# Optimization experiments

Measured on AMD Instinct MI355X. Metric: run time of the kernel, lower is better.

The kernel has to match this reference:

```python
import jax, jax.numpy as jnp
import numpy as np

B, T, H, IN, OUT = 256, 1024, 512, 2, 2


def setup_inputs() -> dict:
    key = jax.random.key(0)
    ks = jax.random.split(key, 12)
    s = 1.0 / np.sqrt(H)
    return {
        "X0": jax.random.normal(ks[0], (B, OUT), jnp.float32),
        "V": jax.random.normal(ks[1], (B, T, IN), jnp.float32),
        # GRU params (torch layout: gates ordered r, z, n)
        "W_ih": jax.random.uniform(ks[2], (3 * H, IN), jnp.float32, -s, s),
        "W_hh": jax.random.uniform(ks[3], (3 * H, H), jnp.float32, -s, s),
        "b_ih": jax.random.uniform(ks[4], (3 * H,), jnp.float32, -s, s),
        "b_hh": jax.random.uniform(ks[5], (3 * H,), jnp.float32, -s, s),
        # attention MLP: Linear(OUT+IN, H//2) -> ReLU -> Linear(H//2, OUT) -> Softmax
        "Wa1": jax.random.uniform(ks[6], (H // 2, OUT + IN), jnp.float32, -s, s),
        "ba1": jax.random.uniform(ks[7], (H // 2,), jnp.float32, -s, s),
        "Wa2": jax.random.uniform(ks[8], (OUT, H // 2), jnp.float32, -s, s),
        "ba2": jax.random.uniform(ks[9], (OUT,), jnp.float32, -s, s),
        # residual layer: Linear(H, OUT)
        "Wr": jax.random.uniform(ks[10], (OUT, H), jnp.float32, -s, s),
        "br": jax.random.uniform(ks[11], (OUT,), jnp.float32, -s, s),
    }


def _forward(X0, V, W_ih, W_hh, b_ih, b_hh, Wa1, ba1, Wa2, ba2, Wr, br):
    # ---- GRU over time (batch_first input, h0 = 0) ----
    # Precompute input projections for all steps: [B, T, 3H]
    gx_all = jnp.einsum('bti,gi->btg', V, W_ih) + b_ih
    gx_tm = jnp.swapaxes(gx_all, 0, 1)  # [T, B, 3H]

    def gru_step(h, gx):
        gh = h @ W_hh.T + b_hh  # [B, 3H]
        r = jax.nn.sigmoid(gx[:, :H] + gh[:, :H])
        z = jax.nn.sigmoid(gx[:, H:2 * H] + gh[:, H:2 * H])
        n = jnp.tanh(gx[:, 2 * H:] + r * gh[:, 2 * H:])
        h_new = (1.0 - z) * n + z * h
        return h_new, h_new

    h0 = jnp.zeros((V.shape[0], H), V.dtype)
    _, h_seq = jax.lax.scan(gru_step, h0, gx_tm)  # [T, B, H]

    # residual_raw = residual_layer(h_t), precomputed for all t: [T, B, OUT]
    res_all = jnp.einsum('tbh,oh->tbo', h_seq, Wr) + br

    v_tm = jnp.swapaxes(V, 0, 1)  # [T, B, IN]; IN == OUT so slice is identity

    def corr_step(x_prev, inp):
        v_t, res_t = inp
        att_in = jnp.concatenate([x_prev, v_t[:, :OUT]], axis=-1)  # [B, OUT+IN]
        hid = jax.nn.relu(att_in @ Wa1.T + ba1)
        aw = jax.nn.softmax(hid @ Wa2.T + ba2, axis=-1)  # [B, OUT]
        x_t = x_prev + v_t[:, :OUT] + aw * res_t
        return x_t, x_t

    _, x_seq = jax.lax.scan(corr_step, X0, (v_tm, res_all))  # [T, B, OUT]
    return jnp.swapaxes(x_seq, 0, 1)  # [B, T, OUT]


def reference(X0, V, W_ih, W_hh, b_ih, b_hh, Wa1, ba1, Wa2, ba2, Wr, br):
    return _forward(X0, V, W_ih, W_hh, b_ih, b_hh, Wa1, ba1, Wa2, ba2, Wr, br)
```

## Files before the change

kernel.cpp:

```cpp
#include <hip/hip_runtime.h>


typedef short bf16x8 __attribute__((ext_vector_type(8)));
typedef float f32x4  __attribute__((ext_vector_type(4)));
typedef unsigned u32x2 __attribute__((ext_vector_type(2)));
typedef unsigned u32x4 __attribute__((ext_vector_type(4)));

__device__ __forceinline__ unsigned f2bf(float f) {
  unsigned u = __builtin_bit_cast(unsigned, f);
  return (u + 0x7fffu + ((u >> 16) & 1u)) >> 16;
}
__device__ __forceinline__ float bf2f(unsigned short u) {
  unsigned v = (unsigned)u << 16;
  return __builtin_bit_cast(float, v);
}

#define KSTEP(kt, areg) \
  acc0 = __builtin_amdgcn_mfma_f32_16x16x32_bf16(areg, wf0[kt], acc0, 0, 0, 0); \
  acc1 = __builtin_amdgcn_mfma_f32_16x16x32_bf16(areg, wf1[kt], acc1, 0, 0, 0); \
  acc2 = __builtin_amdgcn_mfma_f32_16x16x32_bf16(areg, wf2[kt], acc2, 0, 0, 0);

#define PUBA(off, val) \
  asm volatile("global_atomic_swap_x2 %0, %1, off offset:" #off " sc1" \
               :: "v"(pp), "v"(val) : "memory")

__global__ void __launch_bounds__(256, 1) gru_fused(
    const float* __restrict__ V, const float* __restrict__ W_ih,
    const float* __restrict__ W_hh, const float* __restrict__ b_ih,
    const float* __restrict__ b_hh, const float* __restrict__ Wr,
    const float* __restrict__ Wa1, const float* __restrict__ ba1,
    const float* __restrict__ Wa2, const float* __restrict__ ba2v,
    const float* __restrict__ brv, const float* __restrict__ X0,
    float* __restrict__ out,
    char* __restrict__ hbuf)
{
  const int tid  = threadIdx.x;
  const int w    = tid >> 6;
  const int lane = tid & 63;
  const int cl   = lane & 15;
  const int hi4  = lane >> 4;
  const int g    = blockIdx.x & 15;
  const int p    = (blockIdx.x >> 4) & 7;

  __shared__ short hs[2][16][512];
  __shared__ float wrl[2][512];
  __shared__ float wa1l[1024];
  __shared__ float ba1l[256];
  __shared__ float wa2l[2][256];
  char* lds = (char*)hs;

  const int c = p * 64 + w * 16 + cl;

  const float wir0 = W_ih[c * 2 + 0],          wir1 = W_ih[c * 2 + 1];
  const float wiz0 = W_ih[(512 + c) * 2 + 0],  wiz1 = W_ih[(512 + c) * 2 + 1];
  const float win0 = W_ih[(1024 + c) * 2 + 0], win1 = W_ih[(1024 + c) * 2 + 1];
  const float bsr = b_ih[c] + b_hh[c];
  const float bsz = b_ih[512 + c] + b_hh[512 + c];
  const float bin = b_ih[1024 + c];
  const float bhn = b_hh[1024 + c];

  const float ba2_0 = ba2v[0], ba2_1 = ba2v[1];
  const float br0 = brv[0], br1 = brv[1];

  bf16x8 wf0[16], wf1[16], wf2[16];
  #pragma unroll
  for (int gt = 0; gt < 3; ++gt) {
    const float* src = W_hh + ((size_t)(gt * 512 + c)) * 512 + hi4 * 8;
    #pragma unroll
    for (int kt = 0; kt < 16; ++kt) {
      float4 x = *reinterpret_cast<const float4*>(src + kt * 32);
      float4 y = *reinterpret_cast<const float4*>(src + kt * 32 + 4);
      bf16x8 t;
      t[0] = (short)f2bf(x.x); t[1] = (short)f2bf(x.y);
      t[2] = (short)f2bf(x.z); t[3] = (short)f2bf(x.w);
      t[4] = (short)f2bf(y.x); t[5] = (short)f2bf(y.y);
      t[6] = (short)f2bf(y.z); t[7] = (short)f2bf(y.w);
      if (gt == 0) wf0[kt] = t; else if (gt == 1) wf1[kt] = t; else wf2[kt] = t;
    }
  }

  for (int i = tid; i < 8192; i += 256) ((unsigned*)lds)[i] = 0;
  for (int i = tid; i < 512; i += 256) { wrl[0][i] = Wr[i]; wrl[1][i] = Wr[512 + i]; }
  for (int i = tid; i < 1024; i += 256) wa1l[i] = Wa1[i];
  if (tid < 256) { ba1l[tid] = ba1[tid]; wa2l[0][tid] = Wa2[tid]; wa2l[1][tid] = Wa2[256 + tid]; }
  __syncthreads();

  const int urow = tid >> 4, ucol = tid & 15;
  const unsigned roff = (unsigned)(urow * 256 + ucol * 16);

  float h[4] = {0.f, 0.f, 0.f, 0.f};

  float x0 = 0.f, x1 = 0.f;
  if (w < 2) {
    const int gr = g * 16 + 2 * p + w;
    x0 = X0[gr * 2 + 0];
    x1 = X0[gr * 2 + 1];
  }

  auto corr = [&](int sl) {
    const int row = 2 * p + w;
    const int gr  = g * 16 + row;
    const int t   = sl - 1;
    const char* hb = lds + (sl & 1) * 16384 + row * 1024;
    const unsigned off = ((unsigned)(lane * 16)) ^ (((unsigned)row & 7) << 4);
    bf16x8 hv = *(const bf16x8*)(hb + off);
    float r0 = 0.f, r1 = 0.f;
    #pragma unroll
    for (int k2 = 0; k2 < 8; ++k2) {
      float hf = bf2f((unsigned short)hv[k2]);
      r0 += wrl[0][lane * 8 + k2] * hf;
      r1 += wrl[1][lane * 8 + k2] * hf;
    }
    const float2 vt = *reinterpret_cast<const float2*>(&V[((size_t)gr * 1024 + t) * 2]);
    float l0 = 0.f, l1 = 0.f;
    #pragma unroll
    for (int q = 0; q < 4; ++q) {
      const int hh = lane * 4 + q;
      float4 wa = *reinterpret_cast<const float4*>(&wa1l[hh * 4]);
      float hq = wa.x * x0 + wa.y * x1 + wa.z * vt.x + wa.w * vt.y + ba1l[hh];
      hq = fmaxf(hq, 0.f);
      l0 += wa2l[0][hh] * hq;
      l1 += wa2l[1][hh] * hq;
    }
    #pragma unroll
    for (int m = 1; m < 64; m <<= 1) {
      r0 += __shfl_xor(r0, m); r1 += __shfl_xor(r1, m);
      l0 += __shfl_xor(l0, m); l1 += __shfl_xor(l1, m);
    }
    l0 += ba2_0; l1 += ba2_1;
    const float mx = fmaxf(l0, l1);
    const float e0 = __expf(l0 - mx), e1 = __expf(l1 - mx);
    const float inv = 1.f / (e0 + e1);
    x0 += vt.x + (e0 * inv) * (r0 + br0);
    x1 += vt.y + (e1 * inv) * (r1 + br1);
    if (lane == 0) {
      float2 o; o.x = x0; o.y = x1;
      *reinterpret_cast<float2*>(&out[((size_t)gr * 1024 + t) * 2]) = o;
    }
  };

  for (int s = 0; s < 1024; ++s) {
    float2 vv[4];
    #pragma unroll
    for (int j = 0; j < 4; ++j)
      vv[j] = *reinterpret_cast<const float2*>(
          &V[((size_t)(g * 16 + hi4 * 4 + j) * 1024 + (size_t)s) * 2]);

    f32x4 acc0 = {0.f,0.f,0.f,0.f}, acc1 = {0.f,0.f,0.f,0.f}, acc2 = {0.f,0.f,0.f,0.f};
    if (s > 0) {
      const char* ab = lds + (s & 1) * 16384 + cl * 1024;
      const unsigned sw = (unsigned)((cl & 7) << 4);
      #pragma unroll
      for (int kb = 0; kb < 4; ++kb) {
        bf16x8 a0 = *(const bf16x8*)(ab + (((kb * 4 + 0) * 64 + hi4 * 16) ^ sw));
        bf16x8 a1 = *(const bf16x8*)(ab + (((kb * 4 + 1) * 64 + hi4 * 16) ^ sw));
        bf16x8 a2 = *(const bf16x8*)(ab + (((kb * 4 + 2) * 64 + hi4 * 16) ^ sw));
        bf16x8 a3 = *(const bf16x8*)(ab + (((kb * 4 + 3) * 64 + hi4 * 16) ^ sw));
        KSTEP(kb * 4 + 0, a0) KSTEP(kb * 4 + 1, a1)
        KSTEP(kb * 4 + 2, a2) KSTEP(kb * 4 + 3, a3)
      }
    }

    float hn_[4];
    #pragma unroll
    for (int j = 0; j < 4; ++j) {
      float pr = acc0[j] + bsr + wir0 * vv[j].x + wir1 * vv[j].y;
      float pz = acc1[j] + bsz + wiz0 * vv[j].x + wiz1 * vv[j].y;
      float rg = 1.f / (1.f + __expf(-pr));
      float zg = 1.f / (1.f + __expf(-pz));
      float pn = win0 * vv[j].x + win1 * vv[j].y + bin + rg * (acc2[j] + bhn);
      pn = fminf(fmaxf(pn, -30.f), 30.f);
      float e2 = __expf(2.f * pn);
      float tg = (e2 - 1.f) / (e2 + 1.f);
      hn_[j] = (1.f - zg) * tg + zg * h[j];
      h[j] = hn_[j];
    }

    unsigned pk[4];
    #pragma unroll
    for (int j = 0; j < 4; ++j) {
      float o = __shfl_xor(hn_[j], 1);
      pk[j] = f2bf(hn_[j]) | (f2bf(o) << 16);
    }

    if (!(cl & 1)) {
      char* pp = hbuf + (size_t)(s & 1) * 524288 + (size_t)(g * 8 + p) * 4096
               + (unsigned)(hi4 * 4) * 256u + (unsigned)((w * 16 + cl) >> 1) * 8u;
      u32x2 v0, v1, v2, v3;
      v0.x = pk[0]; v0.y = (unsigned)(s + 1);
      v1.x = pk[1]; v1.y = (unsigned)(s + 1);
      v2.x = pk[2]; v2.y = (unsigned)(s + 1);
      v3.x = pk[3]; v3.y = (unsigned)(s + 1);
      PUBA(0, v0); PUBA(256, v1); PUBA(512, v2); PUBA(768, v3);
    }

    if (!(cl & 1)) {
      char* wb = lds + ((s + 1) & 1) * 16384;
      const unsigned bc = (unsigned)(2 * c);
      #pragma unroll
      for (int j = 0; j < 4; ++j) {
        const unsigned row = (unsigned)(hi4 * 4 + j);
        *(unsigned*)(wb + row * 1024 + (bc ^ ((row & 7) << 4))) = pk[j];
      }
    }

    if (s > 0 && w < 2) corr(s);

    {
      char* wb = lds + ((s + 1) & 1) * 16384;
      const unsigned want = (unsigned)(s + 1);
      const char* sbase = hbuf + (size_t)(s & 1) * 524288 + (size_t)(g * 8) * 4096 + roff;
      u32x4 u0, u1, u2, u3, u4, u5, u6;
      unsigned pend = 0x7f;
      if (w >= 2) __builtin_amdgcn_s_sleep(8);
      #define RP(r) ((p + (r) + 1) & 7)
      #define ISSUE(r, ureg) \
        if (pend & (1u << (r))) { \
          const char* src = sbase + RP(r) * 4096; \
          asm volatile("global_load_dwordx4 %0, %1, off sc1" \
                       : "=v"(ureg) : "v"(src) : "memory"); \
        }
      #define HARVEST(r, ureg) \
        if ((pend & (1u << (r))) && ureg.y == want && ureg.w == want) { \
          const unsigned bc = (unsigned)(RP(r) * 128 + ucol * 8); \
          uint2 pay; pay.x = ureg.x; pay.y = ureg.z; \
          *(uint2*)(wb + (unsigned)urow * 1024 + \
                    (bc ^ (((unsigned)urow & 7) << 4))) = pay; \
          pend &= ~(1u << (r)); \
        }
      int gd = 0;
      while (pend) {
        ISSUE(0, u0) ISSUE(1, u1) ISSUE(2, u2) ISSUE(3, u3)
        ISSUE(4, u4) ISSUE(5, u5) ISSUE(6, u6)
        asm volatile("s_waitcnt vmcnt(0)" ::: "memory");
        HARVEST(0, u0) HARVEST(1, u1) HARVEST(2, u2) HARVEST(3, u3)
        HARVEST(4, u4) HARVEST(5, u5) HARVEST(6, u6)
        if (++gd > (1 << 14)) break;
      }
      #undef RP
      #undef ISSUE
      #undef HARVEST
    }
    __syncthreads();
  }

  if (w < 2) corr(1024);
}

extern "C" void kernel_launch(void* const* d_in, const int* in_sizes, int n_in,
                              void* d_out, int out_size, void* d_ws, size_t ws_size,
                              hipStream_t stream) {
  const float* X0   = (const float*)d_in[0];
  const float* V    = (const float*)d_in[1];
  const float* W_ih = (const float*)d_in[2];
  const float* W_hh = (const float*)d_in[3];
  const float* b_ih = (const float*)d_in[4];
  const float* b_hh = (const float*)d_in[5];
  const float* Wa1  = (const float*)d_in[6];
  const float* ba1  = (const float*)d_in[7];
  const float* Wa2  = (const float*)d_in[8];
  const float* ba2  = (const float*)d_in[9];
  const float* Wr   = (const float*)d_in[10];
  const float* br   = (const float*)d_in[11];
  float* out = (float*)d_out;

  char* hbuf = (char*)d_ws;
  hipMemsetAsync(hbuf, 0, 1024 * 1024, stream);

  hipLaunchKernelGGL(gru_fused, dim3(128), dim3(256), 0, stream,
                     V, W_ih, W_hh, b_ih, b_hh, Wr,
                     Wa1, ba1, Wa2, ba2, br, X0, out, hbuf);
}
```

Baseline: 3.190 ms.

## Split gather to waves 2-3 and transpose attention weights in LDS

Waves 0-1 now only run the correction step, and waves 2-3 alone poll the peer blocks' published hidden-state slices, each thread handling two chunks in sequence. This takes the cross-block polling off the correction waves' critical path so the two jobs run concurrently. The attention/residual weights are stored transposed in LDS so each lane reads consecutive addresses, avoiding bank conflicts. The trade-off is that each polling thread serialises twice as many loads, which could lengthen the per-step gather.

```diff
diff --git a/kernel.cpp b/kernel.cpp
--- a/kernel.cpp
+++ b/kernel.cpp
@@ -43,10 +43,10 @@
   const int p    = (blockIdx.x >> 4) & 7;
 
   __shared__ short hs[2][16][512];
-  __shared__ float wrl[2][512];
-  __shared__ float wa1l[1024];
-  __shared__ float ba1l[256];
-  __shared__ float wa2l[2][256];
+  __shared__ float wrt[2][8][64];
+  __shared__ float wa1t[4][4][64];
+  __shared__ float ba1t[4][64];
+  __shared__ float wa2t[2][4][64];
   char* lds = (char*)hs;
 
   const int c = p * 64 + w * 16 + cl;
@@ -80,13 +80,19 @@
   }
 
   for (int i = tid; i < 8192; i += 256) ((unsigned*)lds)[i] = 0;
-  for (int i = tid; i < 512; i += 256) { wrl[0][i] = Wr[i]; wrl[1][i] = Wr[512 + i]; }
-  for (int i = tid; i < 1024; i += 256) wa1l[i] = Wa1[i];
-  if (tid < 256) { ba1l[tid] = ba1[tid]; wa2l[0][tid] = Wa2[tid]; wa2l[1][tid] = Wa2[256 + tid]; }
+  for (int i = tid; i < 512; i += 256) {
+    wrt[0][i & 7][i >> 3] = Wr[i];
+    wrt[1][i & 7][i >> 3] = Wr[512 + i];
+  }
+  for (int i = tid; i < 1024; i += 256) {
+    wa1t[(i >> 2) & 3][i & 3][i >> 4] = Wa1[i];
+  }
+  if (tid < 256) {
+    ba1t[tid & 3][tid >> 2]    = ba1[tid];
+    wa2t[0][tid & 3][tid >> 2] = Wa2[tid];
+    wa2t[1][tid & 3][tid >> 2] = Wa2[256 + tid];
+  }
   __syncthreads();
-
-  const int urow = tid >> 4, ucol = tid & 15;
-  const unsigned roff = (unsigned)(urow * 256 + ucol * 16);
 
   float h[4] = {0.f, 0.f, 0.f, 0.f};
 
@@ -108,19 +114,18 @@
     #pragma unroll
     for (int k2 = 0; k2 < 8; ++k2) {
       float hf = bf2f((unsigned short)hv[k2]);
-      r0 += wrl[0][lane * 8 + k2] * hf;
-      r1 += wrl[1][lane * 8 + k2] * hf;
+      r0 += wrt[0][k2][lane] * hf;
+      r1 += wrt[1][k2][lane] * hf;
     }
     const float2 vt = *reinterpret_cast<const float2*>(&V[((size_t)gr * 1024 + t) * 2]);
     float l0 = 0.f, l1 = 0.f;
     #pragma unroll
     for (int q = 0; q < 4; ++q) {
-      const int hh = lane * 4 + q;
-      float4 wa = *reinterpret_cast<const float4*>(&wa1l[hh * 4]);
-      float hq = wa.x * x0 + wa.y * x1 + wa.z * vt.x + wa.w * vt.y + ba1l[hh];
+      float hq = wa1t[q][0][lane] * x0 + wa1t[q][1][lane] * x1 +
+                 wa1t[q][2][lane] * vt.x + wa1t[q][3][lane] * vt.y + ba1t[q][lane];
       hq = fmaxf(hq, 0.f);
-      l0 += wa2l[0][hh] * hq;
-      l1 += wa2l[1][hh] * hq;
+      l0 += wa2t[0][q][lane] * hq;
+      l1 += wa2t[1][q][lane] * hq;
     }
     #pragma unroll
     for (int m = 1; m < 64; m <<= 1) {
@@ -204,42 +209,49 @@
       }
     }
 
-    if (s > 0 && w < 2) corr(s);
-
-    {
+    if (w < 2) {
+      if (s > 0) corr(s);
+    } else {
       char* wb = lds + ((s + 1) & 1) * 16384;
       const unsigned want = (unsigned)(s + 1);
-      const char* sbase = hbuf + (size_t)(s & 1) * 524288 + (size_t)(g * 8) * 4096 + roff;
-      u32x4 u0, u1, u2, u3, u4, u5, u6;
-      unsigned pend = 0x7f;
-      if (w >= 2) __builtin_amdgcn_s_sleep(8);
+      const char* slot = hbuf + (size_t)(s & 1) * 524288 + (size_t)(g * 8) * 4096;
+      const int local = tid & 127;
+      __builtin_amdgcn_s_sleep(8);
       #define RP(r) ((p + (r) + 1) & 7)
-      #define ISSUE(r, ureg) \
-        if (pend & (1u << (r))) { \
-          const char* src = sbase + RP(r) * 4096; \
-          asm volatile("global_load_dwordx4 %0, %1, off sc1" \
-                       : "=v"(ureg) : "v"(src) : "memory"); \
+      #pragma unroll
+      for (int ci = 0; ci < 2; ++ci) {
+        const int idx = local * 2 + ci;
+        const int ur = idx >> 4, uc = idx & 15;
+        const char* sbase = slot + (unsigned)(ur * 256 + uc * 16);
+        u32x4 u0, u1, u2, u3, u4, u5, u6;
+        unsigned pend = 0x7f;
+        #define ISSUE(r, ureg) \
+          if (pend & (1u << (r))) { \
+            const char* src = sbase + RP(r) * 4096; \
+            asm volatile("global_load_dwordx4 %0, %1, off sc1" \
+                         : "=v"(ureg) : "v"(src) : "memory"); \
+          }
+        #define HARVEST(r, ureg) \
+          if ((pend & (1u << (r))) && ureg.y == want && ureg.w == want) { \
+            const unsigned bc = (unsigned)(RP(r) * 128 + uc * 8); \
+            uint2 pay; pay.x = ureg.x; pay.y = ureg.z; \
+            *(uint2*)(wb + (unsigned)ur * 1024 + \
+                      (bc ^ (((unsigned)ur & 7) << 4))) = pay; \
+            pend &= ~(1u << (r)); \
+          }
+        int gd = 0;
+        while (pend) {
+          ISSUE(0, u0) ISSUE(1, u1) ISSUE(2, u2) ISSUE(3, u3)
+          ISSUE(4, u4) ISSUE(5, u5) ISSUE(6, u6)
+          asm volatile("s_waitcnt vmcnt(0)" ::: "memory");
+          HARVEST(0, u0) HARVEST(1, u1) HARVEST(2, u2) HARVEST(3, u3)
+          HARVEST(4, u4) HARVEST(5, u5) HARVEST(6, u6)
+          if (++gd > (1 << 14)) break;
         }
-      #define HARVEST(r, ureg) \
-        if ((pend & (1u << (r))) && ureg.y == want && ureg.w == want) { \
-          const unsigned bc = (unsigned)(RP(r) * 128 + ucol * 8); \
-          uint2 pay; pay.x = ureg.x; pay.y = ureg.z; \
-          *(uint2*)(wb + (unsigned)urow * 1024 + \
-                    (bc ^ (((unsigned)urow & 7) << 4))) = pay; \
-          pend &= ~(1u << (r)); \
-        }
-      int gd = 0;
-      while (pend) {
-        ISSUE(0, u0) ISSUE(1, u1) ISSUE(2, u2) ISSUE(3, u3)
-        ISSUE(4, u4) ISSUE(5, u5) ISSUE(6, u6)
-        asm volatile("s_waitcnt vmcnt(0)" ::: "memory");
-        HARVEST(0, u0) HARVEST(1, u1) HARVEST(2, u2) HARVEST(3, u3)
-        HARVEST(4, u4) HARVEST(5, u5) HARVEST(6, u6)
-        if (++gd > (1 << 14)) break;
+        #undef ISSUE
+        #undef HARVEST
       }
       #undef RP
-      #undef ISSUE
-      #undef HARVEST
     }
     __syncthreads();
   }
```

After: 3.392 ms. 1.06x slower.
